# Kernel tuning notes

Hardware: AMD Instinct MI355X
Metric: run time of the kernel (lower is better)

The kernel has to match this reference:

```python
import jax, jax.numpy as jnp
import numpy as np
from jax import lax

L = 6        # n_layers
C = 192      # hidden_channels
FC = 768     # filter_channels
H = 2        # n_heads
DK = C // H  # k_channels per head
K = 3        # ffn kernel_size
W = 4        # window_size
B = 4
T = 2048
EPS = 1e-5


def setup_inputs() -> dict:
    key = jax.random.key(0)
    ks = jax.random.split(key, 16)
    def rn(k, shape, scale):
        return jax.random.normal(k, shape, dtype=jnp.float32) * scale
    xavier = (2.0 / (C + C)) ** 0.5
    return {
        "x": jax.random.normal(ks[0], (B, C, T), dtype=jnp.float32),
        "x_mask": jnp.ones((B, 1, T), dtype=jnp.float32),
        "wq": rn(ks[1], (L, C, C), xavier), "bq": jnp.zeros((L, C), jnp.float32),
        "wk": rn(ks[2], (L, C, C), xavier), "bk": jnp.zeros((L, C), jnp.float32),
        "wv": rn(ks[3], (L, C, C), xavier), "bv": jnp.zeros((L, C), jnp.float32),
        "wo": rn(ks[4], (L, C, C), xavier), "bo": jnp.zeros((L, C), jnp.float32),
        "rel_k": rn(ks[5], (L, 1, 2 * W + 1, DK), DK ** -0.5),
        "rel_v": rn(ks[6], (L, 1, 2 * W + 1, DK), DK ** -0.5),
        "ln1_g": jnp.ones((L, C), jnp.float32), "ln1_b": jnp.zeros((L, C), jnp.float32),
        "ffn_w1": rn(ks[7], (L, FC, C, K), 0.02), "ffn_b1": jnp.zeros((L, FC), jnp.float32),
        "ffn_w2": rn(ks[8], (L, C, FC, K), 0.02), "ffn_b2": jnp.zeros((L, C), jnp.float32),
        "ln2_g": jnp.ones((L, C), jnp.float32), "ln2_b": jnp.zeros((L, C), jnp.float32),
    }


def _layer_norm_ch(x, g, b):
    # normalize over channel dim (axis=1) of [B, C, T]
    m = jnp.mean(x, axis=1, keepdims=True)
    v = jnp.mean((x - m) ** 2, axis=1, keepdims=True)
    return g[None, :, None] * (x - m) * lax.rsqrt(v + EPS) + b[None, :, None]


def _conv1x1(x, w, b):
    return jnp.einsum('oc,bct->bot', w, x) + b[None, :, None]


def _conv1d(x, w, b, pad):
    y = lax.conv_general_dilated(x, w, window_strides=(1,), padding=[(pad, pad)],
                                 dimension_numbers=('NCH', 'OIH', 'NCH'))
    return y + b[None, :, None]


def _get_rel(emb, length):
    # emb: [1, 2W+1, DK] -> [1, 2*length-1, DK]
    pad_len = max(length - (W + 1), 0)
    start = max(W + 1 - length, 0)
    emb = jnp.pad(emb, ((0, 0), (pad_len, pad_len), (0, 0)))
    return emb[:, start:start + 2 * length - 1]


def _rel_to_abs(x):
    # [B, H, L, 2L-1] -> [B, H, L, L]
    b, h, l, _ = x.shape
    x = jnp.pad(x, ((0, 0), (0, 0), (0, 0), (0, 1)))
    x = x.reshape(b, h, l * 2 * l)
    x = jnp.pad(x, ((0, 0), (0, 0), (0, l - 1)))
    return x.reshape(b, h, l + 1, 2 * l - 1)[:, :, :l, l - 1:]


def _abs_to_rel(x):
    # [B, H, L, L] -> [B, H, L, 2L-1]
    b, h, l, _ = x.shape
    x = jnp.pad(x, ((0, 0), (0, 0), (0, 0), (0, l - 1)))
    x = x.reshape(b, h, l * (2 * l - 1))
    x = jnp.pad(x, ((0, 0), (0, 0), (l, 0)))
    return x.reshape(b, h, l, 2 * l)[:, :, :, 1:]


def reference(x, x_mask, wq, bq, wk, bk, wv, bv, wo, bo, rel_k, rel_v,
              ln1_g, ln1_b, ffn_w1, ffn_b1, ffn_w2, ffn_b2, ln2_g, ln2_b):
    attn_mask = x_mask[:, :, None, :] * x_mask[:, :, :, None]  # [B,1,T,T]
    x = x * x_mask
    scale = DK ** -0.5
    pad = (K - 1) // 2
    for l in range(L):
        residual = x
        q = _conv1x1(x, wq[l], bq[l]).reshape(B, H, DK, T).transpose(0, 1, 3, 2)
        k = _conv1x1(x, wk[l], bk[l]).reshape(B, H, DK, T).transpose(0, 1, 3, 2)
        v = _conv1x1(x, wv[l], bv[l]).reshape(B, H, DK, T).transpose(0, 1, 3, 2)
        qs = q * scale
        scores = jnp.einsum('bhtd,bhsd->bhts', qs, k)
        rk = _get_rel(rel_k[l], T)[0]  # [2T-1, DK], heads shared
        scores = scores + _rel_to_abs(jnp.einsum('bhtd,md->bhtm', qs, rk))
        scores = jnp.where(attn_mask == 0, jnp.float32(-1e4), scores)
        p = jax.nn.softmax(scores, axis=-1)
        out = jnp.einsum('bhts,bhsd->bhtd', p, v)
        rv = _get_rel(rel_v[l], T)[0]
        out = out + jnp.einsum('bhtm,md->bhtd', _abs_to_rel(p), rv)
        out = out.transpose(0, 1, 3, 2).reshape(B, C, T)
        out = _conv1x1(out, wo[l], bo[l])
        x = _layer_norm_ch(residual + out, ln1_g[l], ln1_b[l])
        residual = x
        h = _conv1d(x * x_mask, ffn_w1[l], ffn_b1[l], pad)
        h = jax.nn.relu(h)  # activation != 'gelu'
        h = _conv1d(h, ffn_w2[l], ffn_b2[l], pad)
        h = h * x_mask
        x = _layer_norm_ch(residual + h, ln2_g[l], ln2_b[l])
    return x * x_mask
```

## Files before the change

kernel.cpp:

```cpp
#include <hip/hip_runtime.h>

#define LNUM 6
#define CH 192
#define FCH 768
#define NH 2
#define DKH 96
#define WIN 4
#define BATCH 4
#define TLEN 2048
#define EPSV 1e-5f
#define SCH 4
#define CHUNK (TLEN / SCH)
#define NBCT (BATCH*CH*TLEN)
#define NBFT (BATCH*FCH*TLEN)
#define BHT (BATCH*NH*TLEN)

typedef __attribute__((ext_vector_type(8))) short bf16x8;
typedef __attribute__((ext_vector_type(4))) float f32x4;
typedef __attribute__((ext_vector_type(8))) unsigned short u16x8;

__device__ __forceinline__ unsigned short f2bf(float f) {
  unsigned int u = __builtin_bit_cast(unsigned int, f);
  u = (u + 0x7fffu + ((u >> 16) & 1u)) >> 16;
  return (unsigned short)u;
}
__device__ __forceinline__ float bf2f(unsigned short s) {
  return __builtin_bit_cast(float, ((unsigned int)s) << 16);
}
__device__ __forceinline__ float exp2a(float x) {
#if __has_builtin(__builtin_amdgcn_exp2f)
  return __builtin_amdgcn_exp2f(x);
#else
  return exp2f(x);
#endif
}

__global__ __launch_bounds__(256) void prep_all(
    const float* __restrict__ wq, const float* __restrict__ wk, const float* __restrict__ wv,
    const float* __restrict__ bq, const float* __restrict__ bk, const float* __restrict__ bv,
    const float* __restrict__ wo, const float* __restrict__ fw1, const float* __restrict__ fw2,
    unsigned short* __restrict__ Wqkv, float* __restrict__ Bqkv,
    unsigned short* __restrict__ Wob, unsigned short* __restrict__ W1b,
    unsigned short* __restrict__ W2b)
{
  const float qscale = 0.10206207261596575f * 1.4426950408889634f;
  const int n0 = LNUM * 576 * CH;
  const int n1 = LNUM * CH * CH;
  const int n2 = LNUM * 3 * FCH * CH;
  const int n3 = LNUM * 3 * CH * FCH;
  int total = n0 + n1 + n2 + n3;
  for (int i = blockIdx.x * 256 + threadIdx.x; i < total; i += gridDim.x * 256) {
    if (i < n0) {
      int c = i % CH; int n = (i / CH) % 576; int l = i / (CH * 576);
      float sc = (n < 192) ? qscale : 1.f;
      const float* src = (n < 192) ? wq : (n < 384) ? wk : wv;
      int nn = n % 192;
      Wqkv[i] = f2bf(src[((size_t)l * CH + nn) * CH + c] * sc);
      if (c == 0) {
        const float* bs = (n < 192) ? bq : (n < 384) ? bk : bv;
        Bqkv[l * 576 + n] = bs[l * CH + nn] * sc;
      }
    } else if (i < n0 + n1) {
      int j = i - n0;
      Wob[j] = f2bf(wo[j]);
    } else if (i < n0 + n1 + n2) {
      int j = i - n0 - n1;
      int c = j % CH; int t1 = j / CH;
      int f = t1 % FCH; int t2 = t1 / FCH;
      int kk = t2 % 3; int l = t2 / 3;
      W1b[j] = f2bf(fw1[(((size_t)l * FCH + f) * CH + c) * 3 + kk]);
    } else {
      int j = i - n0 - n1 - n2;
      int c = j % FCH; int t1 = j / FCH;
      int f = t1 % CH; int t2 = t1 / CH;
      int kk = t2 % 3; int l = t2 / 3;
      W2b[j] = f2bf(fw2[(((size_t)l * CH + f) * FCH + c) * 3 + kk]);
    }
  }
}

__global__ __launch_bounds__(256) void tin_kernel(const float* __restrict__ x,
    const float* __restrict__ mask, float* __restrict__ Xc, unsigned short* __restrict__ Xbf) {
  __shared__ float ls[32][33];
  int b = blockIdx.z; int c0 = blockIdx.y * 32, t0 = blockIdx.x * 32;
  int tx = threadIdx.x & 31, ty = threadIdx.x >> 5;
  #pragma unroll
  for (int j = 0; j < 4; ++j)
    ls[ty + j * 8][tx] = x[((size_t)b * CH + c0 + ty + j * 8) * TLEN + t0 + tx];
  __syncthreads();
  #pragma unroll
  for (int j = 0; j < 4; ++j) {
    int t = t0 + ty + j * 8;
    float v = ls[tx][ty + j * 8] * mask[b * TLEN + t];
    size_t o = ((size_t)b * TLEN + t) * CH + c0 + tx;
    Xc[o] = v; Xbf[o] = f2bf(v);
  }
}

__global__ __launch_bounds__(256) void tout_kernel(const float* __restrict__ Xc,
    const float* __restrict__ mask, float* __restrict__ out) {
  __shared__ float ls[32][33];
  int b = blockIdx.z; int c0 = blockIdx.y * 32, t0 = blockIdx.x * 32;
  int tx = threadIdx.x & 31, ty = threadIdx.x >> 5;
  #pragma unroll
  for (int j = 0; j < 4; ++j)
    ls[ty + j * 8][tx] = Xc[((size_t)b * TLEN + t0 + ty + j * 8) * CH + c0 + tx];
  __syncthreads();
  #pragma unroll
  for (int j = 0; j < 4; ++j)
    out[((size_t)b * CH + c0 + ty + j * 8) * TLEN + t0 + tx] =
        ls[tx][ty + j * 8] * mask[b * TLEN + t0 + tx];
}

template<int OUTMODE, int NSHIFT, int RELU, int KSPLIT, int MFR>
__global__ __launch_bounds__(256) void gemm_tc(
    const unsigned short* __restrict__ A, const unsigned short* __restrict__ Bw,
    const float* __restrict__ bias, void* __restrict__ Y, int Cin, int N)
{
  constexpr int HALO = (NSHIFT == 3) ? 1 : 0;
  constexpr int AROWS = MFR * 32 + 2 * HALO;
  constexpr int ACH = (AROWS * 8 + 255) / 256;
  constexpr int BCH = (NSHIFT * 64 * 8) / 256;
  __shared__ __align__(16) unsigned short As[AROWS][72];
  __shared__ __align__(16) unsigned short Bs[NSHIFT][64][72];
  int zz = blockIdx.z;
  int b = zz / KSPLIT, ks = zz % KSPLIT;
  int t0 = blockIdx.x * (MFR * 32), n0 = blockIdx.y * 64;
  int tid = threadIdx.x;
  int w = tid >> 6, lane = tid & 63;
  int wr = w >> 1, wc = w & 1;
  int lr = lane & 15, lg = lane >> 4;
  const unsigned short* Ab = A + (size_t)b * TLEN * Cin;
  int klen = Cin / KSPLIT, k0 = ks * klen;

  int ar[ACH], ac8[ACH]; bool aok[ACH], ain[ACH];
  #pragma unroll
  for (int j = 0; j < ACH; ++j) {
    int f = tid + j * 256;
    ar[j] = f >> 3; ac8[j] = (f & 7) * 8;
    aok[j] = (f < AROWS * 8);
    int tg = t0 - HALO + ar[j];
    ain[j] = aok[j] && (!HALO || (tg >= 0 && tg < TLEN));
  }
  int brr[BCH], bkk[BCH], bc8[BCH];
  #pragma unroll
  for (int j = 0; j < BCH; ++j) {
    int f = tid + j * 256;
    bkk[j] = f >> 9; brr[j] = (f >> 3) & 63; bc8[j] = (f & 7) * 8;
  }

  u16x8 areg[ACH], breg[BCH];
  f32x4 acc[MFR][2] = {};

  #pragma unroll
  for (int j = 0; j < ACH; ++j) {
    u16x8 v = {};
    if (ain[j]) v = *(const u16x8*)&Ab[(size_t)(t0 - HALO + ar[j]) * Cin + k0 + ac8[j]];
    areg[j] = v;
  }
  #pragma unroll
  for (int j = 0; j < BCH; ++j)
    breg[j] = *(const u16x8*)&Bw[((size_t)bkk[j] * N + n0 + brr[j]) * Cin + k0 + bc8[j]];

  for (int kc = k0; kc < k0 + klen; kc += 64) {
    __syncthreads();
    #pragma unroll
    for (int j = 0; j < ACH; ++j)
      if (aok[j]) *(u16x8*)&As[ar[j]][ac8[j]] = areg[j];
    #pragma unroll
    for (int j = 0; j < BCH; ++j)
      *(u16x8*)&Bs[bkk[j]][brr[j]][bc8[j]] = breg[j];
    if (kc + 64 < k0 + klen) {
      int kn = kc + 64;
      #pragma unroll
      for (int j = 0; j < ACH; ++j) {
        u16x8 v = {};
        if (ain[j]) v = *(const u16x8*)&Ab[(size_t)(t0 - HALO + ar[j]) * Cin + kn + ac8[j]];
        areg[j] = v;
      }
      #pragma unroll
      for (int j = 0; j < BCH; ++j)
        breg[j] = *(const u16x8*)&Bw[((size_t)bkk[j] * N + n0 + brr[j]) * Cin + kn + bc8[j]];
    }
    __syncthreads();
    #pragma unroll
    for (int kk = 0; kk < NSHIFT; ++kk) {
      #pragma unroll
      for (int k2 = 0; k2 < 2; ++k2) {
        bf16x8 b0 = *(const bf16x8*)&Bs[kk][wc * 32 + lr][k2 * 32 + lg * 8];
        bf16x8 b1 = *(const bf16x8*)&Bs[kk][wc * 32 + 16 + lr][k2 * 32 + lg * 8];
        #pragma unroll
        for (int i = 0; i < MFR; ++i) {
          bf16x8 a = *(const bf16x8*)&As[wr * MFR * 16 + i * 16 + lr + kk][k2 * 32 + lg * 8];
          acc[i][0] = __builtin_amdgcn_mfma_f32_16x16x32_bf16(a, b0, acc[i][0], 0, 0, 0);
          acc[i][1] = __builtin_amdgcn_mfma_f32_16x16x32_bf16(a, b1, acc[i][1], 0, 0, 0);
        }
      }
    }
  }
  #pragma unroll
  for (int i = 0; i < MFR; ++i) {
    #pragma unroll
    for (int j = 0; j < 2; ++j) {
      int n = n0 + wc * 32 + j * 16 + lr;
      float bb = (ks == 0) ? bias[n] : 0.f;
      float vals[4];
      #pragma unroll
      for (int r = 0; r < 4; ++r) {
        float v = acc[i][j][r] + bb;
        if (RELU) v = fmaxf(v, 0.f);
        vals[r] = v;
      }
      int trow = t0 + wr * MFR * 16 + i * 16 + lg * 4;
      if (OUTMODE == 0) {
        unsigned short* Yp = (unsigned short*)Y + ((size_t)b * TLEN + trow) * N + n;
        #pragma unroll
        for (int r = 0; r < 4; ++r) Yp[(size_t)r * N] = f2bf(vals[r]);
      } else if (OUTMODE == 2) {
        float* Yp = (float*)Y + (size_t)ks * NBCT + ((size_t)b * TLEN + trow) * N + n;
        #pragma unroll
        for (int r = 0; r < 4; ++r) Yp[(size_t)r * N] = vals[r];
      } else {
        unsigned short* base = (unsigned short*)Y;
        if (n0 < 192) {
          unsigned short* Yp = base + ((size_t)b * TLEN + trow) * CH + n;
          #pragma unroll
          for (int r = 0; r < 4; ++r) Yp[(size_t)r * CH] = f2bf(vals[r]);
        } else if (n0 < 384) {
          unsigned short* Yp = base + (size_t)NBCT + ((size_t)b * TLEN + trow) * CH + (n - 192);
          #pragma unroll
          for (int r = 0; r < 4; ++r) Yp[(size_t)r * CH] = f2bf(vals[r]);
        } else {
          ushort4 pk;
          pk.x = f2bf(vals[0]); pk.y = f2bf(vals[1]); pk.z = f2bf(vals[2]); pk.w = f2bf(vals[3]);
          *(ushort4*)(base + 2 * (size_t)NBCT + ((size_t)b * CH + (n - 384)) * TLEN + trow) = pk;
        }
      }
    }
  }
}

template<int NY>
__global__ __launch_bounds__(256) void ln_cl_kernel(
    const float* __restrict__ res, const float* __restrict__ y0,
    const float* __restrict__ y1, const float* __restrict__ g,
    const float* __restrict__ bt, float* __restrict__ Xc, unsigned short* __restrict__ Xbf)
{
  int row = blockIdx.x * 4 + (threadIdx.x >> 6);
  int lane = threadIdx.x & 63;
  const float* r = res + (size_t)row * CH;
  const float* ya = y0 + (size_t)row * CH;
  const float* yb = (NY == 2) ? y1 + (size_t)row * CH : nullptr;
  float v[3]; float s = 0.f, s2 = 0.f;
  #pragma unroll
  for (int j = 0; j < 3; ++j) {
    float t = r[lane + 64 * j] + ya[lane + 64 * j];
    if (NY == 2) t += yb[lane + 64 * j];
    v[j] = t; s += t; s2 += t * t;
  }
  #pragma unroll
  for (int m = 1; m <= 32; m <<= 1) {
    s += __shfl_xor(s, m, 64);
    s2 += __shfl_xor(s2, m, 64);
  }
  float mean = s * (1.f / CH);
  float var = s2 * (1.f / CH) - mean * mean;
  float rs = rsqrtf(var + EPSV);
  #pragma unroll
  for (int j = 0; j < 3; ++j) {
    int c = lane + 64 * j;
    float o = g[c] * (v[j] - mean) * rs + bt[c];
    size_t idx = (size_t)row * CH + c;
    Xc[idx] = o; Xbf[idx] = f2bf(o);
  }
}

__global__ __launch_bounds__(256, 4) void flash_part(
    const unsigned short* __restrict__ Qg, const unsigned short* __restrict__ Kg,
    const unsigned short* __restrict__ Vg, const float* __restrict__ relk,
    float* __restrict__ Opart, float* __restrict__ mG, float* __restrict__ lG,
    float* __restrict__ bandG)
{
  __shared__ __align__(16) unsigned short KsB[64 * 104];
  __shared__ __align__(16) unsigned short QV[96 * 72];
  __shared__ __align__(16) unsigned short Ps[64][72];
  __shared__ float qrk[64][9];
  int bh = blockIdx.y; int b = bh >> 1, h = bh & 1;
  int t0 = blockIdx.x * 64;
  int c0 = blockIdx.z * CHUNK;
  int tid = threadIdx.x; int w = tid >> 6, lane = tid & 63;
  int lr = lane & 15, lg = lane >> 4;
  int q = w * 16 + lr;
  const unsigned short* Qb = Qg + (size_t)b * TLEN * CH + h * DKH;
  const unsigned short* Kb = Kg + (size_t)b * TLEN * CH + h * DKH;
  const unsigned short* Vb = Vg + ((size_t)b * CH + h * DKH) * TLEN;
  unsigned short (*Qs)[104] = (unsigned short(*)[104])QV;
  unsigned short (*Vs)[72] = (unsigned short(*)[72])QV;
  unsigned short (*Ks)[104] = (unsigned short(*)[104])KsB;

  int kr[3], kc8[3], vr[3], vc8[3];
  #pragma unroll
  for (int j = 0; j < 3; ++j) {
    int f = tid + j * 256;
    kr[j] = f / 12; kc8[j] = (f % 12) * 8;
    vr[j] = f >> 3; vc8[j] = (f & 7) * 8;
  }

  for (int f = tid; f < 64 * 12; f += 256) {
    int r = f / 12, c8 = (f % 12) * 8;
    *(u16x8*)&Qs[r][c8] = *(const u16x8*)&Qb[(size_t)(t0 + r) * CH + c8];
  }
  __syncthreads();
  bool overlap = (t0 + 64 + WIN > c0) && (t0 - WIN < c0 + CHUNK);
  if (overlap) {
    for (int f = tid; f < 576; f += 256) {
      int r = f / 9, dd = f - (f / 9) * 9;
      float s = 0.f;
      #pragma unroll 8
      for (int d = 0; d < DKH; ++d) s += bf2f(Qs[r][d]) * relk[dd * DKH + d];
      qrk[r][dd] = s;
    }
  }
  bf16x8 qf[3];
  #pragma unroll
  for (int kc = 0; kc < 3; ++kc) qf[kc] = *(const bf16x8*)&Qs[q][kc * 32 + lg * 8];
  float mrow = -1e30f, lrow = 0.f;
  f32x4 oacc[6] = {};

  u16x8 kreg[3], vreg[3];
  #pragma unroll
  for (int j = 0; j < 3; ++j)
    kreg[j] = *(const u16x8*)&Kb[(size_t)(c0 + kr[j]) * CH + kc8[j]];
  #pragma unroll
  for (int j = 0; j < 3; ++j)
    vreg[j] = *(const u16x8*)&Vb[(size_t)vr[j] * TLEN + c0 + vc8[j]];

  for (int it = 0; it < CHUNK / 64; ++it) {
    int s0 = c0 + it * 64;
    __syncthreads();
    #pragma unroll
    for (int j = 0; j < 3; ++j) *(u16x8*)&Ks[kr[j]][kc8[j]] = kreg[j];
    #pragma unroll
    for (int j = 0; j < 3; ++j) *(u16x8*)&Vs[vr[j]][vc8[j]] = vreg[j];
    if (it + 1 < CHUNK / 64) {
      int sn = s0 + 64;
      #pragma unroll
      for (int j = 0; j < 3; ++j)
        kreg[j] = *(const u16x8*)&Kb[(size_t)(sn + kr[j]) * CH + kc8[j]];
      #pragma unroll
      for (int j = 0; j < 3; ++j)
        vreg[j] = *(const u16x8*)&Vb[(size_t)vr[j] * TLEN + sn + vc8[j]];
    }
    __syncthreads();

    f32x4 sacc[4] = {};
    __builtin_amdgcn_s_setprio(1);
    #pragma unroll
    for (int kc = 0; kc < 3; ++kc) {
      #pragma unroll
      for (int ct = 0; ct < 4; ++ct) {
        bf16x8 kfr = *(const bf16x8*)&Ks[ct * 16 + lr][kc * 32 + lg * 8];
        sacc[ct] = __builtin_amdgcn_mfma_f32_16x16x32_bf16(kfr, qf[kc], sacc[ct], 0, 0, 0);
      }
    }
    __builtin_amdgcn_s_setprio(0);
    if (s0 + 64 + WIN > t0 && s0 < t0 + 64 + WIN) {
      #pragma unroll
      for (int ct = 0; ct < 4; ++ct)
        #pragma unroll
        for (int r = 0; r < 4; ++r) {
          int dlt = (s0 + ct * 16 + lg * 4 + r) - (t0 + q);
          if (dlt >= -WIN && dlt <= WIN) {
            float v = sacc[ct][r] + qrk[q][dlt + WIN];
            sacc[ct][r] = v;
            bandG[((size_t)bh * TLEN + t0 + q) * 9 + dlt + WIN] = v;
          }
        }
    }
    float cm[4];
    #pragma unroll
    for (int ct = 0; ct < 4; ++ct)
      cm[ct] = fmaxf(fmaxf(sacc[ct][0], sacc[ct][1]), fmaxf(sacc[ct][2], sacc[ct][3]));
    float tmax = fmaxf(fmaxf(cm[0], cm[1]), fmaxf(cm[2], cm[3]));
    tmax = fmaxf(tmax, __shfl_xor(tmax, 16, 64));
    tmax = fmaxf(tmax, __shfl_xor(tmax, 32, 64));
    bool upd = !__all(tmax <= mrow + 8.f);
    float mnew = upd ? fmaxf(mrow, tmax) : mrow;
    float psum = 0.f;
    #pragma unroll
    for (int ct = 0; ct < 4; ++ct) {
      float p0 = exp2a(sacc[ct][0] - mnew), p1 = exp2a(sacc[ct][1] - mnew);
      float p2 = exp2a(sacc[ct][2] - mnew), p3 = exp2a(sacc[ct][3] - mnew);
      psum += (p0 + p1) + (p2 + p3);
      ushort4 pk;
      pk.x = f2bf(p0); pk.y = f2bf(p1); pk.z = f2bf(p2); pk.w = f2bf(p3);
      *(ushort4*)&Ps[q][ct * 16 + lg * 4] = pk;
    }
    psum += __shfl_xor(psum, 16, 64);
    psum += __shfl_xor(psum, 32, 64);
    if (upd) {
      float alpha = exp2a(mrow - mnew);
      lrow *= alpha;
      float alo[4];
      #pragma unroll
      for (int r = 0; r < 4; ++r) alo[r] = __shfl(alpha, lg * 4 + r, 64);
      #pragma unroll
      for (int dt = 0; dt < 6; ++dt)
        #pragma unroll
        for (int r = 0; r < 4; ++r) oacc[dt][r] *= alo[r];
      mrow = mnew;
    }
    lrow += psum;
    __builtin_amdgcn_s_setprio(1);
    #pragma unroll
    for (int ks = 0; ks < 2; ++ks) {
      bf16x8 pa = *(const bf16x8*)&Ps[q][ks * 32 + lg * 8];
      #pragma unroll
      for (int dt = 0; dt < 6; ++dt) {
        bf16x8 vf = *(const bf16x8*)&Vs[dt * 16 + lr][ks * 32 + lg * 8];
        oacc[dt] = __builtin_amdgcn_mfma_f32_16x16x32_bf16(pa, vf, oacc[dt], 0, 0, 0);
      }
    }
    __builtin_amdgcn_s_setprio(0);
  }

  size_t pbase = ((size_t)blockIdx.z * (BATCH * NH) + bh) * TLEN + t0;
  #pragma unroll
  for (int dt = 0; dt < 6; ++dt)
    #pragma unroll
    for (int r = 0; r < 4; ++r)
      Opart[(pbase + w * 16 + lg * 4 + r) * 96 + dt * 16 + lr] = oacc[dt][r];
  if (lg == 0) {
    mG[pbase + q] = mrow;
    lG[pbase + q] = lrow;
  }
}

__global__ __launch_bounds__(256) void flash_combine(
    const float* __restrict__ Opart, const float* __restrict__ mG,
    const float* __restrict__ lG, const float* __restrict__ bandG,
    const float* __restrict__ relv, unsigned short* __restrict__ AO)
{
  int sub = threadIdx.x >> 7;
  int d = threadIdx.x & 127;
  int row = blockIdx.x * 2 + sub;
  int bh = row >> 11, t = row & 2047;
  float mv[SCH], lv[SCH], m = -1e30f;
  #pragma unroll
  for (int c = 0; c < SCH; ++c) {
    mv[c] = mG[(size_t)c * BHT + row];
    lv[c] = lG[(size_t)c * BHT + row];
    m = fmaxf(m, mv[c]);
  }
  float L = 0.f, e[SCH];
  #pragma unroll
  for (int c = 0; c < SCH; ++c) { e[c] = exp2a(mv[c] - m); L += lv[c] * e[c]; }
  if (d < 96) {
    float acc = 0.f;
    #pragma unroll
    for (int c = 0; c < SCH; ++c)
      acc += Opart[((size_t)c * BHT + row) * 96 + d] * e[c];
    #pragma unroll
    for (int dd = 0; dd < 9; ++dd) {
      int s = t + dd - WIN;
      if (s >= 0 && s < TLEN)
        acc += exp2a(bandG[(size_t)row * 9 + dd] - m) * relv[dd * 96 + d];
    }
    int b = bh >> 1, h = bh & 1;
    AO[((size_t)b * TLEN + t) * CH + h * DKH + d] = f2bf(acc / L);
  }
}

extern "C" void kernel_launch(void* const* d_in, const int* in_sizes, int n_in,
                              void* d_out, int out_size, void* d_ws, size_t ws_size,
                              hipStream_t stream) {
  (void)in_sizes; (void)n_in; (void)out_size; (void)ws_size;
  const float* x    = (const float*)d_in[0];
  const float* mask = (const float*)d_in[1];
  const float* wq   = (const float*)d_in[2];
  const float* bq   = (const float*)d_in[3];
  const float* wk   = (const float*)d_in[4];
  const float* bk   = (const float*)d_in[5];
  const float* wv   = (const float*)d_in[6];
  const float* bv   = (const float*)d_in[7];
  const float* wo   = (const float*)d_in[8];
  const float* bo   = (const float*)d_in[9];
  const float* relk = (const float*)d_in[10];
  const float* relv = (const float*)d_in[11];
  const float* ln1g = (const float*)d_in[12];
  const float* ln1b = (const float*)d_in[13];
  const float* fw1  = (const float*)d_in[14];
  const float* fb1  = (const float*)d_in[15];
  const float* fw2  = (const float*)d_in[16];
  const float* fb2  = (const float*)d_in[17];
  const float* ln2g = (const float*)d_in[18];
  const float* ln2b = (const float*)d_in[19];

  char* p = (char*)d_ws;
  float* Xc = (float*)p;                      p += (size_t)NBCT * 4;
  unsigned short* Xbf  = (unsigned short*)p;  p += (size_t)NBCT * 2;
  unsigned short* Qbf  = (unsigned short*)p;  p += (size_t)NBCT * 2;
  unsigned short* Kbf  = (unsigned short*)p;  p += (size_t)NBCT * 2;
  unsigned short* Vbf  = (unsigned short*)p;  p += (size_t)NBCT * 2;
  unsigned short* AObf = (unsigned short*)p;  p += (size_t)NBCT * 2;
  char* R = p;                                p += (size_t)NBCT * 8 + (size_t)NBFT * 2;
  float* Yo  = (float*)R;
  float* Opart = (float*)R;
  unsigned short* Hbf = (unsigned short*)(R + (size_t)NBCT * 8);
  float* mG = (float*)p;                      p += (size_t)SCH * BHT * 4;
  float* lG = (float*)p;                      p += (size_t)SCH * BHT * 4;
  float* bandG = (float*)p;                   p += (size_t)BHT * 9 * 4;
  unsigned short* Wqkv = (unsigned short*)p;  p += (size_t)LNUM * 576 * CH * 2;
  float* Bqkv = (float*)p;                    p += (size_t)LNUM * 576 * 4;
  unsigned short* Wob  = (unsigned short*)p;  p += (size_t)LNUM * CH * CH * 2;
  unsigned short* W1b  = (unsigned short*)p;  p += (size_t)LNUM * 3 * FCH * CH * 2;
  unsigned short* W2b  = (unsigned short*)p;

  prep_all<<<2048, 256, 0, stream>>>(wq, wk, wv, bq, bk, bv, wo, fw1, fw2,
                                     Wqkv, Bqkv, Wob, W1b, W2b);
  tin_kernel<<<dim3(TLEN / 32, CH / 32, BATCH), 256, 0, stream>>>(x, mask, Xc, Xbf);

  for (int l = 0; l < LNUM; ++l) {
    gemm_tc<3, 1, 0, 1, 4><<<dim3(16, 9, 4), 256, 0, stream>>>(
        Xbf, Wqkv + (size_t)l * 576 * CH, Bqkv + l * 576, Qbf, CH, 576);
    flash_part<<<dim3(32, 8, SCH), 256, 0, stream>>>(
        Qbf, Kbf, Vbf, relk + (size_t)l * 9 * DKH, Opart, mG, lG, bandG);
    flash_combine<<<BHT / 2, 256, 0, stream>>>(
        Opart, mG, lG, bandG, relv + (size_t)l * 9 * DKH, AObf);
    gemm_tc<2, 1, 0, 1, 2><<<dim3(32, 3, 4), 256, 0, stream>>>(
        AObf, Wob + (size_t)l * CH * CH, bo + l * CH, Yo, CH, CH);
    ln_cl_kernel<1><<<BATCH * TLEN / 4, 256, 0, stream>>>(
        Xc, Yo, nullptr, ln1g + l * CH, ln1b + l * CH, Xc, Xbf);
    gemm_tc<0, 3, 1, 1, 4><<<dim3(16, 12, 4), 256, 0, stream>>>(
        Xbf, W1b + (size_t)l * 3 * FCH * CH, fb1 + l * FCH, Hbf, CH, FCH);
    gemm_tc<2, 3, 0, 2, 2><<<dim3(32, 3, 8), 256, 0, stream>>>(
        Hbf, W2b + (size_t)l * 3 * CH * FCH, fb2 + l * CH, Yo, FCH, CH);
    ln_cl_kernel<2><<<BATCH * TLEN / 4, 256, 0, stream>>>(
        Xc, Yo, Yo + NBCT, ln2g + l * CH, ln2b + l * CH, Xc, Xbf);
  }
  tout_kernel<<<dim3(TLEN / 32, CH / 32, BATCH), 256, 0, stream>>>(Xc, mask, (float*)d_out);
}
```

Baseline: 656.8 us.

## Write bf16 GEMM outputs for O-proj and FFN2, drop split-K partials

The output-projection and second FFN GEMMs now write bf16 results directly instead of fp32 (previously with a split-K of 2 for FFN2 producing two fp32 partials). The layer-norm kernel reads a single bf16 tensor, which cuts global memory traffic for the intermediate outputs and removes the partial summation. The GEMM tile config changes to smaller M tiles with more blocks to keep parallelism without split-K. The cost is reduced precision of the residual-add input and a longer K loop per block for FFN2.

```diff
diff --git a/kernel.cpp b/kernel.cpp
--- a/kernel.cpp
+++ b/kernel.cpp
@@ -216,10 +216,6 @@
         unsigned short* Yp = (unsigned short*)Y + ((size_t)b * TLEN + trow) * N + n;
         #pragma unroll
         for (int r = 0; r < 4; ++r) Yp[(size_t)r * N] = f2bf(vals[r]);
-      } else if (OUTMODE == 2) {
-        float* Yp = (float*)Y + (size_t)ks * NBCT + ((size_t)b * TLEN + trow) * N + n;
-        #pragma unroll
-        for (int r = 0; r < 4; ++r) Yp[(size_t)r * N] = vals[r];
       } else {
         unsigned short* base = (unsigned short*)Y;
         if (n0 < 192) {
@@ -240,22 +236,19 @@
   }
 }
 
-template<int NY>
 __global__ __launch_bounds__(256) void ln_cl_kernel(
-    const float* __restrict__ res, const float* __restrict__ y0,
-    const float* __restrict__ y1, const float* __restrict__ g,
-    const float* __restrict__ bt, float* __restrict__ Xc, unsigned short* __restrict__ Xbf)
+    const float* __restrict__ res, const unsigned short* __restrict__ yb,
+    const float* __restrict__ g, const float* __restrict__ bt,
+    float* __restrict__ Xc, unsigned short* __restrict__ Xbf)
 {
   int row = blockIdx.x * 4 + (threadIdx.x >> 6);
   int lane = threadIdx.x & 63;
   const float* r = res + (size_t)row * CH;
-  const float* ya = y0 + (size_t)row * CH;
-  const float* yb = (NY == 2) ? y1 + (size_t)row * CH : nullptr;
+  const unsigned short* y = yb + (size_t)row * CH;
   float v[3]; float s = 0.f, s2 = 0.f;
   #pragma unroll
   for (int j = 0; j < 3; ++j) {
-    float t = r[lane + 64 * j] + ya[lane + 64 * j];
-    if (NY == 2) t += yb[lane + 64 * j];
+    float t = r[lane + 64 * j] + bf2f(y[lane + 64 * j]);
     v[j] = t; s += t; s2 += t * t;
   }
   #pragma unroll
@@ -503,10 +496,10 @@
   unsigned short* Kbf  = (unsigned short*)p;  p += (size_t)NBCT * 2;
   unsigned short* Vbf  = (unsigned short*)p;  p += (size_t)NBCT * 2;
   unsigned short* AObf = (unsigned short*)p;  p += (size_t)NBCT * 2;
-  char* R = p;                                p += (size_t)NBCT * 8 + (size_t)NBFT * 2;
-  float* Yo  = (float*)R;
+  char* R = p;                                p += (size_t)NBCT * 16;
   float* Opart = (float*)R;
-  unsigned short* Hbf = (unsigned short*)(R + (size_t)NBCT * 8);
+  unsigned short* Ybf = (unsigned short*)R;
+  unsigned short* Hbf = (unsigned short*)(R + (size_t)NBCT * 2);
   float* mG = (float*)p;                      p += (size_t)SCH * BHT * 4;
   float* lG = (float*)p;                      p += (size_t)SCH * BHT * 4;
   float* bandG = (float*)p;                   p += (size_t)BHT * 9 * 4;
@@ -527,16 +520,16 @@
         Qbf, Kbf, Vbf, relk + (size_t)l * 9 * DKH, Opart, mG, lG, bandG);
     flash_combine<<<BHT / 2, 256, 0, stream>>>(
         Opart, mG, lG, bandG, relv + (size_t)l * 9 * DKH, AObf);
-    gemm_tc<2, 1, 0, 1, 2><<<dim3(32, 3, 4), 256, 0, stream>>>(
-        AObf, Wob + (size_t)l * CH * CH, bo + l * CH, Yo, CH, CH);
-    ln_cl_kernel<1><<<BATCH * TLEN / 4, 256, 0, stream>>>(
-        Xc, Yo, nullptr, ln1g + l * CH, ln1b + l * CH, Xc, Xbf);
+    gemm_tc<0, 1, 0, 1, 1><<<dim3(64, 3, 4), 256, 0, stream>>>(
+        AObf, Wob + (size_t)l * CH * CH, bo + l * CH, Ybf, CH, CH);
+    ln_cl_kernel<<<BATCH * TLEN / 4, 256, 0, stream>>>(
+        Xc, Ybf, ln1g + l * CH, ln1b + l * CH, Xc, Xbf);
     gemm_tc<0, 3, 1, 1, 4><<<dim3(16, 12, 4), 256, 0, stream>>>(
         Xbf, W1b + (size_t)l * 3 * FCH * CH, fb1 + l * FCH, Hbf, CH, FCH);
-    gemm_tc<2, 3, 0, 2, 2><<<dim3(32, 3, 8), 256, 0, stream>>>(
-        Hbf, W2b + (size_t)l * 3 * CH * FCH, fb2 + l * CH, Yo, FCH, CH);
-    ln_cl_kernel<2><<<BATCH * TLEN / 4, 256, 0, stream>>>(
-        Xc, Yo, Yo + NBCT, ln2g + l * CH, ln2b + l * CH, Xc, Xbf);
+    gemm_tc<0, 3, 0, 1, 1><<<dim3(64, 3, 4), 256, 0, stream>>>(
+        Hbf, W2b + (size_t)l * 3 * CH * FCH, fb2 + l * CH, Ybf, FCH, CH);
+    ln_cl_kernel<<<BATCH * TLEN / 4, 256, 0, stream>>>(
+        Xc, Ybf, ln2g + l * CH, ln2b + l * CH, Xc, Xbf);
   }
   tout_kernel<<<dim3(TLEN / 32, CH / 32, BATCH), 256, 0, stream>>>(Xc, mask, (float*)d_out);
 }
```

Measured after the change: 663.8 us. About the same (+1.1%).
